# Kernel tuning notes

Hardware: AMD Instinct MI355X
Metric: run time of the kernel (lower is better)

Reference implementation:

```python
import jax, jax.numpy as jnp
import numpy as np

B, N, K, HID, L, OUT, HEADS = 2, 512, 30, 128, 3, 400, 4
FF = 4 * HID


def gather_nodes(nodes, idx):
    # nodes [B,N,C], idx [B,N,K] -> [B,N,K,C]
    return jax.vmap(lambda n, i: n[i])(nodes, idx)


def cat_edge_endpoints(h_E, h_V, E_idx):
    # h_i uses E_idx[:,:,0] (self node) broadcast over K, h_j gathers neighbors
    idx_i = jnp.broadcast_to(E_idx[:, :, :1], E_idx.shape)
    h_i = gather_nodes(h_V, idx_i)
    h_j = gather_nodes(h_V, E_idx)
    return jnp.concatenate([h_i, h_j, h_E], axis=-1)  # [B,N,K,3*HID]


def norm(x, g, b, eps=1e-6):
    # Ingraham-style Normalize: unbiased var, eps added to sigma too
    mu = x.mean(-1, keepdims=True)
    sigma = jnp.sqrt(x.var(-1, keepdims=True, ddof=1) + eps)
    return g * (x - mu) / (sigma + eps) + b


def edge_attention(h_E, h_EV, wq, wk, wv, wo, mask_attend):
    b, n, k, H = h_E.shape
    d = H // HEADS
    Q = (h_E @ wq).reshape(b, n, k, HEADS, d).transpose(0, 1, 3, 2, 4)   # [B,N,h,K,d]
    Kk = (h_EV @ wk).reshape(b, n, k, HEADS, d).transpose(0, 1, 3, 2, 4)
    Vv = (h_EV @ wv).reshape(b, n, k, HEADS, d).transpose(0, 1, 3, 2, 4)
    logits = jnp.einsum('bnhqd,bnhkd->bnhqk', Q, Kk) / np.float32(np.sqrt(d))
    m = mask_attend[:, :, None, :, None]                 # [B,N,1,K,1]
    mask = m * jnp.swapaxes(m, -1, -2)                   # [B,N,1,K,K]
    logits = jnp.where(mask > 0, logits, jnp.finfo(jnp.float32).min)
    attend = jax.nn.softmax(logits, axis=-1) * mask
    upd = jnp.einsum('bnhqk,bnhkd->bnhqd', attend, Vv)
    upd = upd.transpose(0, 1, 3, 2, 4).reshape(b, n, k, H)
    return upd @ wo


def merge_duplicate_edges(hE, E_idx):
    # scatter edges into dense [B,N,N,H], transpose, gather reverse edge, average
    b, n, k, h = hE.shape
    bi = jnp.arange(b)[:, None, None]
    ni = jnp.arange(n)[None, :, None]
    coll = jnp.zeros((b, n, n, h), hE.dtype).at[bi, ni, E_idx].set(hE)
    rev = coll.transpose(0, 2, 1, 3)[bi, ni, E_idx]
    return (hE + rev) / 2


def setup_inputs() -> dict:
    key = jax.random.key(0)
    ks = iter(jax.random.split(key, 32))

    def xav(k, shape):
        fan_in, fan_out = shape[-2], shape[-1]
        return jax.random.normal(k, shape, jnp.float32) * np.float32(np.sqrt(2.0 / (fan_in + fan_out)))

    V = jax.random.normal(next(ks), (B, N, HID), jnp.float32)
    E = jax.random.normal(next(ks), (B, N, K, HID), jnp.float32)
    x_mask = jnp.ones((B, N), jnp.float32)
    E_idx = jax.random.randint(next(ks), (B, N, K), 0, N)
    # slot 0 is the self edge, as in k-NN graphs
    E_idx = E_idx.at[:, :, 0].set(jnp.arange(N)[None, :])
    inp = dict(V=V, E=E, x_mask=x_mask, E_idx=E_idx)
    inp['Wv_w'] = xav(next(ks), (HID, HID)); inp['Wv_b'] = jnp.zeros((HID,), jnp.float32)
    inp['We_w'] = xav(next(ks), (HID, HID)); inp['We_b'] = jnp.zeros((HID,), jnp.float32)
    inp['WQ'] = xav(next(ks), (L, HID, HID))
    inp['WK'] = xav(next(ks), (L, 3 * HID, HID))
    inp['WV'] = xav(next(ks), (L, 3 * HID, HID))
    inp['WO'] = xav(next(ks), (L, HID, HID))
    inp['ln1_g'] = jnp.ones((L, HID), jnp.float32); inp['ln1_b'] = jnp.zeros((L, HID), jnp.float32)
    inp['ln2_g'] = jnp.ones((L, HID), jnp.float32); inp['ln2_b'] = jnp.zeros((L, HID), jnp.float32)
    inp['ff1_w'] = xav(next(ks), (L, HID, FF)); inp['ff1_b'] = jnp.zeros((L, FF), jnp.float32)
    inp['ff2_w'] = xav(next(ks), (L, FF, HID)); inp['ff2_b'] = jnp.zeros((L, HID), jnp.float32)
    inp['Wout_w'] = xav(next(ks), (HID, OUT)); inp['Wout_b'] = jnp.zeros((OUT,), jnp.float32)
    return inp


def reference(V, E, x_mask, E_idx, Wv_w, Wv_b, We_w, We_b, WQ, WK, WV, WO,
              ln1_g, ln1_b, ln2_g, ln2_b, ff1_w, ff1_b, ff2_w, ff2_b,
              Wout_w, Wout_b):
    h_V = V @ Wv_w + Wv_b                                   # [B,N,HID]
    h_E = E @ We_w + We_b                                   # [B,N,K,HID]
    mask_attend = gather_nodes(x_mask[..., None], E_idx)[..., 0] * x_mask[..., None]
    for l in range(L):
        h_EV = cat_edge_endpoints(h_E, h_V, E_idx)          # [B,N,K,3*HID]
        dh = edge_attention(h_E, h_EV, WQ[l], WK[l], WV[l], WO[l], mask_attend)
        h_E = norm(h_E + dh, ln1_g[l], ln1_b[l])
        dh = jnp.maximum(h_E @ ff1_w[l] + ff1_b[l], 0.0) @ ff2_w[l] + ff2_b[l]
        h_E = norm(h_E + dh, ln2_g[l], ln2_b[l])
        h_E = h_E * x_mask[:, :, None, None]                # mask_E
    h_out = h_E @ Wout_w + Wout_b                           # [B,N,K,OUT]
    return merge_duplicate_edges(h_out, E_idx)
```

## Files before the change

### kernel.cpp

```cpp
#include <hip/hip_runtime.h>

#define NB 512
#define KNB 30
#define HID 128
#define NL 3
#define NOUT 400
#define NFF 512

typedef _Float16 f16;
typedef _Float16 f16x8 __attribute__((ext_vector_type(8)));
typedef _Float16 f16x4 __attribute__((ext_vector_type(4)));
typedef float f32x4 __attribute__((ext_vector_type(4)));

#define MFMA16(a, b, c) __builtin_amdgcn_mfma_f32_16x16x32_f16(a, b, c, 0, 0, 0)

#define PK_WE   0
#define PK_WQ   16384
#define PK_WK   65536
#define PK_WV   114688
#define PK_WO   163840
#define PK_F1   212992
#define PK_F2   409600
#define PK_WOUT 606208
#define PK_TOTAL 657408

__global__ void k_hv(const float* __restrict__ V, const float* __restrict__ Wv,
                     const float* __restrict__ bv, float* __restrict__ hV) {
  int idx = blockIdx.x * 256 + threadIdx.x;
  int row = idx >> 7, c = idx & 127;
  const float* vr = V + row * HID;
  float acc = bv[c];
  for (int i = 0; i < HID; ++i) acc = fmaf(vr[i], Wv[i * HID + c], acc);
  hV[idx] = acc;
}

__global__ void k_tables(const float* __restrict__ hV, const float* __restrict__ WK,
                         const float* __restrict__ WVp, float* __restrict__ tbl) {
  int idx = blockIdx.x * 256 + threadIdx.x;
  int c = idx & 127;
  int row = (idx >> 7) & 1023;
  int t = idx >> 17;
  int l = t >> 2, part = t & 3;
  const float* W;
  if (part == 0)      W = WK  + l * 3 * HID * HID;
  else if (part == 1) W = WK  + l * 3 * HID * HID + HID * HID;
  else if (part == 2) W = WVp + l * 3 * HID * HID;
  else                W = WVp + l * 3 * HID * HID + HID * HID;
  const float* hr = hV + row * HID;
  float acc = 0.f;
  for (int i = 0; i < HID; ++i) acc = fmaf(hr[i], W[i * HID + c], acc);
  tbl[idx] = acc;
}

__device__ __forceinline__ void pack_one(const float* W, int N, int r, f16* dst) {
  int j = r & 7, l = (r >> 3) & 63, t = r >> 9;
  int NT = N >> 4;
  int nt = t % NT, ks = t / NT;
  int k = ks * 32 + ((l >> 4) << 3) + j;
  int c = nt * 16 + (l & 15);
  dst[r] = (f16)W[k * N + c];
}

__global__ void k_pack(const float* __restrict__ We, const float* __restrict__ WQ,
                       const float* __restrict__ WK, const float* __restrict__ WV,
                       const float* __restrict__ WO, const float* __restrict__ f1w,
                       const float* __restrict__ f2w, const float* __restrict__ Wout,
                       f16* __restrict__ P) {
  int idx = blockIdx.x * 256 + threadIdx.x;
  if (idx >= PK_TOTAL) return;
  const float* W; int N; int r; f16* dst;
  if (idx < 212992) {
    int s = idx >> 14; r = idx & 16383; N = 128;
    dst = P + (idx - r);
    if (s == 0) W = We;
    else if (s < 4) W = WQ + (s - 1) * 16384;
    else if (s < 7) W = WK + (s - 4) * 49152 + 32768;
    else if (s < 10) W = WV + (s - 7) * 49152 + 32768;
    else W = WO + (s - 10) * 16384;
  } else if (idx < 409600) {
    int t = (idx - 212992) >> 16; r = (idx - 212992) & 65535;
    W = f1w + t * 65536; N = 512; dst = P + 212992 + t * 65536;
  } else if (idx < 606208) {
    int t = (idx - 409600) >> 16; r = (idx - 409600) & 65535;
    W = f2w + t * 65536; N = 128; dst = P + 409600 + t * 65536;
  } else {
    r = idx - 606208; W = Wout; N = 400; dst = P + 606208;
  }
  pack_one(W, N, r, dst);
}

__device__ __forceinline__ void mfma_block8(const f16* Ab, int astr, const f16x8* B,
                                            int nt0, int nt1, f32x4 acc[2][2],
                                            int ln, int g, int lane) {
  f16x8 af[2][4];
#pragma unroll
  for (int mt = 0; mt < 2; ++mt)
#pragma unroll
    for (int ks = 0; ks < 4; ++ks)
      af[mt][ks] = *(const f16x8*)&Ab[(mt * 16 + ln) * astr + ks * 32 + g * 8];
#pragma unroll
  for (int ks = 0; ks < 4; ++ks) {
    f16x8 b0 = B[(ks * 8 + nt0) * 64 + lane];
    f16x8 b1 = B[(ks * 8 + nt1) * 64 + lane];
#pragma unroll
    for (int mt = 0; mt < 2; ++mt) {
      acc[mt][0] = MFMA16(af[mt][ks], b0, acc[mt][0]);
      acc[mt][1] = MFMA16(af[mt][ks], b1, acc[mt][1]);
    }
  }
}

__device__ __forceinline__ void layer_norm_cvt(float (*hEp)[132], f16* hEhp,
                                               const float* __restrict__ gg,
                                               const float* __restrict__ bb,
                                               float mmul, int tid) {
  int r = tid >> 3, g8 = tid & 7;
  if (r < KNB) {
    float x[16]; float s1 = 0.f, s2 = 0.f;
    int cb = g8 * 16;
#pragma unroll
    for (int m = 0; m < 16; ++m) { x[m] = hEp[r][cb + m]; s1 += x[m]; s2 += x[m] * x[m]; }
#pragma unroll
    for (int o = 1; o < 8; o <<= 1) { s1 += __shfl_xor(s1, o); s2 += __shfl_xor(s2, o); }
    float mu = s1 * (1.f / 128.f);
    float var = fmaf(-s1, mu, s2) * (1.f / 127.f);
    float inv = 1.f / (sqrtf(var + 1e-6f) + 1e-6f);
    f16x8 h0, h1;
#pragma unroll
    for (int m = 0; m < 16; ++m) {
      int c = cb + m;
      float y = (gg[c] * (x[m] - mu) * inv + bb[c]) * mmul;
      hEp[r][c] = y;
      if (m < 8) h0[m] = (f16)y; else h1[m - 8] = (f16)y;
    }
    *(f16x8*)&hEhp[r * 136 + cb] = h0;
    *(f16x8*)&hEhp[r * 136 + cb + 8] = h1;
  }
}

__launch_bounds__(256, 2)
__global__ void k_main(
    const float* __restrict__ E, const int* __restrict__ Eix, const float* __restrict__ xm,
    const float* __restrict__ be,
    const float* __restrict__ l1g, const float* __restrict__ l1b,
    const float* __restrict__ l2g, const float* __restrict__ l2b,
    const float* __restrict__ f1b, const float* __restrict__ f2b,
    const float* __restrict__ bout,
    const f16* __restrict__ P, const float* __restrict__ tbl,
    float* __restrict__ gOUT) {
  __shared__ __align__(16) char SM[63744];
  float (*hE)[132] = (float(*)[132])SM;
  f16* hEh = (f16*)(SM + 16896);
  char* poolB = SM + 25600;
  f16* Qh   = (f16*)(poolB);
  f16* Kh   = (f16*)(poolB + 8704);
  f16* Vt   = (f16*)(poolB + 17408);
  f16* atth = (f16*)(poolB + 27648);
  f16* hidh = (f16*)(poolB);
  float* ma = (float*)(SM + 63488);
  int* eidx = (int*)(SM + 63616);

  const int tid = threadIdx.x;
  const int bid = blockIdx.x;
  const int b = bid >> 9, n = bid & (NB - 1);
  const int lane = tid & 63, wv = tid >> 6;
  const int ln = lane & 15, g = lane >> 4;

  {
    float4 z = make_float4(0.f, 0.f, 0.f, 0.f);
    float4* p = (float4*)(SM + 16896);
    for (int x = tid; x < 2912; x += 256) p[x] = z;
  }
  if (tid < 32) {
    int e = (tid < KNB) ? Eix[(b * NB + n) * KNB + tid] : 0;
    eidx[tid] = e;
    float mr = xm[b * NB + n];
    ma[tid] = (tid < KNB) ? mr * xm[b * NB + e] : 0.f;
  }
  __syncthreads();
  {
    const float4* Eg = (const float4*)(E + (size_t)(b * NB + n) * KNB * HID);
    for (int x = tid; x < 960; x += 256) {
      float4 e4 = Eg[x];
      int r = x >> 5, c = (x & 31) << 2;
      f16x4 h; h[0] = (f16)e4.x; h[1] = (f16)e4.y; h[2] = (f16)e4.z; h[3] = (f16)e4.w;
      *(f16x4*)&hEh[r * 136 + c] = h;
    }
  }
  const float mrow = xm[b * NB + n];
  __syncthreads();

  {
    f32x4 acc[2][2] = {};
    mfma_block8(hEh, 136, (const f16x8*)(P + PK_WE), wv, wv + 4, acc, ln, g, lane);
    __syncthreads();
#pragma unroll
    for (int nts = 0; nts < 2; ++nts) {
      int c = (wv + nts * 4) * 16 + ln;
      float bev = be[c];
#pragma unroll
      for (int mt = 0; mt < 2; ++mt)
#pragma unroll
        for (int i = 0; i < 4; ++i) {
          int r = mt * 16 + 4 * g + i;
          if (r < KNB) {
            float v = acc[mt][nts][i] + bev;
            hE[r][c] = v;
            hEh[r * 136 + c] = (f16)v;
          }
        }
    }
  }
  __syncthreads();

  for (int l = 0; l < NL; ++l) {
    const f16x8* PQ = (const f16x8*)(P + PK_WQ + l * 16384);
    const f16x8* PKk = (const f16x8*)(P + PK_WK + l * 16384);
    const f16x8* PV = (const f16x8*)(P + PK_WV + l * 16384);
    const f16x8* PO = (const f16x8*)(P + PK_WO + l * 16384);
    const f16x8* P1 = (const f16x8*)(P + PK_F1 + l * 65536);
    const f16x8* P2 = (const f16x8*)(P + PK_F2 + l * 65536);
    const float* Ki = tbl + (size_t)(l * 4 + 0) * (2 * NB * HID) + (size_t)b * NB * HID;
    const float* Kj = tbl + (size_t)(l * 4 + 1) * (2 * NB * HID) + (size_t)b * NB * HID;
    const float* Vi = tbl + (size_t)(l * 4 + 2) * (2 * NB * HID) + (size_t)b * NB * HID;
    const float* Vj = tbl + (size_t)(l * 4 + 3) * (2 * NB * HID) + (size_t)b * NB * HID;

    {
      int e0v = eidx[0];
      int er[2][4];
#pragma unroll
      for (int mt = 0; mt < 2; ++mt)
#pragma unroll
        for (int i = 0; i < 4; ++i) er[mt][i] = eidx[mt * 16 + 4 * g + i];
      float kib[2], vib[2], kjv[2][2][4], vjv[2][2][4];
#pragma unroll
      for (int nts = 0; nts < 2; ++nts) {
        int c = (wv + nts * 4) * 16 + ln;
        kib[nts] = Ki[e0v * 128 + c];
        vib[nts] = Vi[e0v * 128 + c];
#pragma unroll
        for (int mt = 0; mt < 2; ++mt)
#pragma unroll
          for (int i = 0; i < 4; ++i) {
            kjv[nts][mt][i] = Kj[er[mt][i] * 128 + c];
            vjv[nts][mt][i] = Vj[er[mt][i] * 128 + c];
          }
      }
      f32x4 qa[2][2] = {}, kk[2][2] = {}, va[2][2] = {};
      mfma_block8(hEh, 136, PQ, wv, wv + 4, qa, ln, g, lane);
      mfma_block8(hEh, 136, PKk, wv, wv + 4, kk, ln, g, lane);
      mfma_block8(hEh, 136, PV, wv, wv + 4, va, ln, g, lane);
#pragma unroll
      for (int nts = 0; nts < 2; ++nts) {
        int c = (wv + nts * 4) * 16 + ln;
#pragma unroll
        for (int mt = 0; mt < 2; ++mt)
#pragma unroll
          for (int i = 0; i < 4; ++i) {
            int r = mt * 16 + 4 * g + i;
            Qh[r * 136 + c] = (f16)qa[mt][nts][i];
            Kh[r * 136 + c] = (f16)(kk[mt][nts][i] + kib[nts] + kjv[nts][mt][i]);
            Vt[c * 40 + r]  = (f16)(va[mt][nts][i] + vib[nts] + vjv[nts][mt][i]);
          }
      }
    }
    __syncthreads();

    {
      int h = wv;
      f16* ath = atth + h * 1280;
      f16x8 qf[2], kf[2];
#pragma unroll
      for (int mt = 0; mt < 2; ++mt)
        qf[mt] = *(const f16x8*)&Qh[(mt * 16 + ln) * 136 + h * 32 + g * 8];
#pragma unroll
      for (int nt = 0; nt < 2; ++nt)
        kf[nt] = *(const f16x8*)&Kh[(nt * 16 + ln) * 136 + h * 32 + g * 8];
      f32x4 s[2][2] = {};
#pragma unroll
      for (int mt = 0; mt < 2; ++mt)
#pragma unroll
        for (int nt = 0; nt < 2; ++nt) s[mt][nt] = MFMA16(qf[mt], kf[nt], s[mt][nt]);
      float mk0 = ma[ln], mk1 = ma[16 + ln];
      const float scale = 0.17677669529663687f;
#pragma unroll
      for (int mt = 0; mt < 2; ++mt) {
#pragma unroll
        for (int i = 0; i < 4; ++i) {
          int q = mt * 16 + 4 * g + i;
          float mq = ma[q];
          float v0 = s[mt][0][i] * scale;
          float v1 = s[mt][1][i] * scale;
          v0 = (mq * mk0 > 0.f) ? v0 : -3.4028234663852886e38f;
          v1 = (mq * mk1 > 0.f) ? v1 : -3.4028234663852886e38f;
          float mx = fmaxf(v0, v1);
          mx = fmaxf(mx, __shfl_xor(mx, 1));
          mx = fmaxf(mx, __shfl_xor(mx, 2));
          mx = fmaxf(mx, __shfl_xor(mx, 4));
          mx = fmaxf(mx, __shfl_xor(mx, 8));
          float e0 = __expf(v0 - mx), e1 = __expf(v1 - mx);
          float sm = e0 + e1;
          sm += __shfl_xor(sm, 1); sm += __shfl_xor(sm, 2);
          sm += __shfl_xor(sm, 4); sm += __shfl_xor(sm, 8);
          float inv = 1.f / sm;
          ath[q * 40 + ln]      = (f16)(e0 * inv * (mq * mk0));
          ath[q * 40 + 16 + ln] = (f16)(e1 * inv * (mq * mk1));
        }
      }
      asm volatile("s_waitcnt lgkmcnt(0)" ::: "memory");
      __builtin_amdgcn_sched_barrier(0);
      f32x4 u[2][2] = {};
      f16x8 aat[2], vbf[2];
#pragma unroll
      for (int mt = 0; mt < 2; ++mt)
        aat[mt] = *(const f16x8*)&ath[(mt * 16 + ln) * 40 + g * 8];
#pragma unroll
      for (int nt = 0; nt < 2; ++nt)
        vbf[nt] = *(const f16x8*)&Vt[((2 * h + nt) * 16 + ln) * 40 + g * 8];
#pragma unroll
      for (int mt = 0; mt < 2; ++mt)
#pragma unroll
        for (int nt = 0; nt < 2; ++nt) u[mt][nt] = MFMA16(aat[mt], vbf[nt], u[mt][nt]);
#pragma unroll
      for (int mt = 0; mt < 2; ++mt)
#pragma unroll
        for (int nt = 0; nt < 2; ++nt)
#pragma unroll
          for (int i = 0; i < 4; ++i) {
            int r = mt * 16 + 4 * g + i;
            hEh[r * 136 + h * 32 + nt * 16 + ln] = (f16)u[mt][nt][i];
          }
    }
    __syncthreads();

    {
      f32x4 acc[2][2] = {};
      mfma_block8(hEh, 136, PO, wv, wv + 4, acc, ln, g, lane);
#pragma unroll
      for (int nts = 0; nts < 2; ++nts) {
        int c = (wv + nts * 4) * 16 + ln;
#pragma unroll
        for (int mt = 0; mt < 2; ++mt)
#pragma unroll
          for (int i = 0; i < 4; ++i) {
            int r = mt * 16 + 4 * g + i;
            if (r < KNB) hE[r][c] += acc[mt][nts][i];
          }
      }
    }
    __syncthreads();
    layer_norm_cvt(hE, hEh, l1g + l * HID, l1b + l * HID, 1.f, tid);
    __syncthreads();

    {
      f16x8 af[2][4];
#pragma unroll
      for (int mt = 0; mt < 2; ++mt)
#pragma unroll
        for (int ks = 0; ks < 4; ++ks)
          af[mt][ks] = *(const f16x8*)&hEh[(mt * 16 + ln) * 136 + ks * 32 + g * 8];
      f32x4 acc[2][8] = {};
#pragma unroll
      for (int ks = 0; ks < 4; ++ks)
#pragma unroll
        for (int t = 0; t < 8; ++t) {
          f16x8 bv = P1[(ks * 32 + wv + 4 * t) * 64 + lane];
          acc[0][t] = MFMA16(af[0][ks], bv, acc[0][t]);
          acc[1][t] = MFMA16(af[1][ks], bv, acc[1][t]);
        }
      const float* b1 = f1b + l * NFF;
#pragma unroll
      for (int t = 0; t < 8; ++t) {
        int c = (wv + 4 * t) * 16 + ln;
        float b1v = b1[c];
#pragma unroll
        for (int mt = 0; mt < 2; ++mt)
#pragma unroll
          for (int i = 0; i < 4; ++i) {
            int r = mt * 16 + 4 * g + i;
            hidh[r * 520 + c] = (f16)fmaxf(acc[mt][t][i] + b1v, 0.f);
          }
      }
    }
    __syncthreads();

    {
      f32x4 acc[2][2] = {};
#pragma unroll
      for (int ks = 0; ks < 16; ++ks) {
        f16x8 a0 = *(const f16x8*)&hidh[ln * 520 + ks * 32 + g * 8];
        f16x8 a1 = *(const f16x8*)&hidh[(16 + ln) * 520 + ks * 32 + g * 8];
        f16x8 b0 = P2[(ks * 8 + wv) * 64 + lane];
        f16x8 b1 = P2[(ks * 8 + wv + 4) * 64 + lane];
        acc[0][0] = MFMA16(a0, b0, acc[0][0]);
        acc[0][1] = MFMA16(a0, b1, acc[0][1]);
        acc[1][0] = MFMA16(a1, b0, acc[1][0]);
        acc[1][1] = MFMA16(a1, b1, acc[1][1]);
      }
      const float* b2 = f2b + l * HID;
#pragma unroll
      for (int nts = 0; nts < 2; ++nts) {
        int c = (wv + nts * 4) * 16 + ln;
        float b2v = b2[c];
#pragma unroll
        for (int mt = 0; mt < 2; ++mt)
#pragma unroll
          for (int i = 0; i < 4; ++i) {
            int r = mt * 16 + 4 * g + i;
            if (r < KNB) hE[r][c] += acc[mt][nts][i] + b2v;
          }
      }
    }
    __syncthreads();
    layer_norm_cvt(hE, hEh, l2g + l * HID, l2b + l * HID, mrow, tid);
    __syncthreads();
  }

  {
    float* gO = gOUT + (size_t)((b * NB + n) * KNB) * NOUT;
    f16x8 af[2][4];
#pragma unroll
    for (int mt = 0; mt < 2; ++mt)
#pragma unroll
      for (int ks = 0; ks < 4; ++ks)
        af[mt][ks] = *(const f16x8*)&hEh[(mt * 16 + ln) * 136 + ks * 32 + g * 8];
    const f16x8* PW = (const f16x8*)(P + PK_WOUT);
#pragma unroll
    for (int mt = 0; mt < 2; ++mt) {
      for (int nt = wv; nt < 25; nt += 4) {
        f32x4 acc = {};
#pragma unroll
        for (int ks = 0; ks < 4; ++ks) {
          f16x8 bv = PW[(ks * 25 + nt) * 64 + lane];
          acc = MFMA16(af[mt][ks], bv, acc);
        }
        int c = nt * 16 + ln;
        float bo = bout[c];
#pragma unroll
        for (int i = 0; i < 4; ++i) {
          int r = mt * 16 + 4 * g + i;
          if (r < KNB) gO[r * 400 + c] = acc[i] + bo;
        }
      }
    }
  }
}

__global__ void k_clearT(int* __restrict__ T) {
  int i = blockIdx.x * 256 + threadIdx.x;
  if (i < 2 * NB * NB) T[i] = 0;
}
__global__ void k_buildT(const int* __restrict__ Eix, int* __restrict__ T) {
  int idx = blockIdx.x * 256 + threadIdx.x;
  if (idx < 2 * NB * KNB) {
    int b = idx / (NB * KNB);
    int rem = idx % (NB * KNB);
    int i = rem / KNB, k = rem % KNB;
    int j = Eix[idx];
    atomicMax(&T[(b * NB + i) * NB + j], k + 1);
  }
}
__global__ void k_merge(const float* __restrict__ HO, const int* __restrict__ Eix,
                        const int* __restrict__ T, float* __restrict__ out) {
  int gid = blockIdx.x * 256 + threadIdx.x;
  if (gid >= 2 * NB * KNB * (NOUT / 4)) return;
  int c4 = gid % (NOUT / 4);
  int bnk = gid / (NOUT / 4);
  int b = bnk / (NB * KNB);
  int n = (bnk / KNB) % NB;
  int j = Eix[bnk];
  int kp = T[(b * NB + j) * NB + n];
  float4 a = ((const float4*)HO)[(size_t)bnk * (NOUT / 4) + c4];
  float4 rv = make_float4(0.f, 0.f, 0.f, 0.f);
  if (kp > 0) rv = ((const float4*)HO)[(size_t)((b * NB + j) * KNB + (kp - 1)) * (NOUT / 4) + c4];
  ((float4*)out)[gid] = make_float4(0.5f * (a.x + rv.x), 0.5f * (a.y + rv.y),
                                    0.5f * (a.z + rv.z), 0.5f * (a.w + rv.w));
}

extern "C" void kernel_launch(void* const* d_in, const int* in_sizes, int n_in,
                              void* d_out, int out_size, void* d_ws, size_t ws_size,
                              hipStream_t stream) {
  const float* V   = (const float*)d_in[0];
  const float* E   = (const float*)d_in[1];
  const float* xmk = (const float*)d_in[2];
  const int*   Eix = (const int*)d_in[3];
  const float* Wv  = (const float*)d_in[4];
  const float* bv  = (const float*)d_in[5];
  const float* We  = (const float*)d_in[6];
  const float* be  = (const float*)d_in[7];
  const float* WQ  = (const float*)d_in[8];
  const float* WK  = (const float*)d_in[9];
  const float* WVp = (const float*)d_in[10];
  const float* WO  = (const float*)d_in[11];
  const float* l1g = (const float*)d_in[12];
  const float* l1b = (const float*)d_in[13];
  const float* l2g = (const float*)d_in[14];
  const float* l2b = (const float*)d_in[15];
  const float* f1w = (const float*)d_in[16];
  const float* f1b = (const float*)d_in[17];
  const float* f2w = (const float*)d_in[18];
  const float* f2b = (const float*)d_in[19];
  const float* Wou = (const float*)d_in[20];
  const float* bou = (const float*)d_in[21];

  float* HO  = (float*)d_ws;
  float* tbl = HO + 12288000ull;
  float* hV  = tbl + 1572864ull;
  f16*   P   = (f16*)(hV + 131072ull);
  int*   T   = (int*)tbl;

  k_hv<<<512, 256, 0, stream>>>(V, Wv, bv, hV);
  k_tables<<<6144, 256, 0, stream>>>(hV, WK, WVp, tbl);
  k_pack<<<2568, 256, 0, stream>>>(We, WQ, WK, WVp, WO, f1w, f2w, Wou, P);
  k_main<<<1024, 256, 0, stream>>>(E, Eix, xmk, be, l1g, l1b, l2g, l2b,
                                   f1b, f2b, bou, P, tbl, HO);
  k_clearT<<<2048, 256, 0, stream>>>(T);
  k_buildT<<<120, 256, 0, stream>>>(Eix, T);
  k_merge<<<12000, 256, 0, stream>>>(HO, Eix, T, (float*)d_out);
}
```

Measured before the change: 342.7 us.

## Restructure k_main to two waves owning 16-row slabs with register-resident residual

Reworks the main edge kernel from 4 waves splitting output columns into 2 waves each owning 16 edge rows across all 128 columns. The residual stream now stays in registers and layer norm runs on those registers with shuffle reductions, which removes the fp32 shared-memory copy and most block barriers. The FFN is chunked so the 512-wide hidden layer is produced and consumed in 128-column pieces through a small per-wave buffer. The cost is fewer threads per block, higher register pressure, and each wave reloading every weight fragment, which may lower occupancy or raise global/L2 traffic.

Result: slower. 575.1 us (+67.8%).

```diff
diff --git a/kernel.cpp b/kernel.cpp
--- a/kernel.cpp
+++ b/kernel.cpp
@@ -13,6 +13,7 @@
 typedef float f32x4 __attribute__((ext_vector_type(4)));
 
 #define MFMA16(a, b, c) __builtin_amdgcn_mfma_f32_16x16x32_f16(a, b, c, 0, 0, 0)
+#define FLTMIN -3.4028234663852886e38f
 
 #define PK_WE   0
 #define PK_WQ   16384
@@ -89,56 +90,39 @@
   pack_one(W, N, r, dst);
 }
 
-__device__ __forceinline__ void mfma_block8(const f16* Ab, int astr, const f16x8* B,
-                                            int nt0, int nt1, f32x4 acc[2][2],
-                                            int ln, int g, int lane) {
-  f16x8 af[2][4];
-#pragma unroll
-  for (int mt = 0; mt < 2; ++mt)
-#pragma unroll
-    for (int ks = 0; ks < 4; ++ks)
-      af[mt][ks] = *(const f16x8*)&Ab[(mt * 16 + ln) * astr + ks * 32 + g * 8];
-#pragma unroll
-  for (int ks = 0; ks < 4; ++ks) {
-    f16x8 b0 = B[(ks * 8 + nt0) * 64 + lane];
-    f16x8 b1 = B[(ks * 8 + nt1) * 64 + lane];
-#pragma unroll
-    for (int mt = 0; mt < 2; ++mt) {
-      acc[mt][0] = MFMA16(af[mt][ks], b0, acc[mt][0]);
-      acc[mt][1] = MFMA16(af[mt][ks], b1, acc[mt][1]);
-    }
-  }
-}
-
-__device__ __forceinline__ void layer_norm_cvt(float (*hEp)[132], f16* hEhp,
-                                               const float* __restrict__ gg,
-                                               const float* __restrict__ bb,
-                                               float mmul, int tid) {
-  int r = tid >> 3, g8 = tid & 7;
-  if (r < KNB) {
-    float x[16]; float s1 = 0.f, s2 = 0.f;
-    int cb = g8 * 16;
-#pragma unroll
-    for (int m = 0; m < 16; ++m) { x[m] = hEp[r][cb + m]; s1 += x[m]; s2 += x[m] * x[m]; }
-#pragma unroll
-    for (int o = 1; o < 8; o <<= 1) { s1 += __shfl_xor(s1, o); s2 += __shfl_xor(s2, o); }
-    float mu = s1 * (1.f / 128.f);
-    float var = fmaf(-s1, mu, s2) * (1.f / 127.f);
-    float inv = 1.f / (sqrtf(var + 1e-6f) + 1e-6f);
-    f16x8 h0, h1;
-#pragma unroll
-    for (int m = 0; m < 16; ++m) {
-      int c = cb + m;
-      float y = (gg[c] * (x[m] - mu) * inv + bb[c]) * mmul;
-      hEp[r][c] = y;
-      if (m < 8) h0[m] = (f16)y; else h1[m - 8] = (f16)y;
-    }
-    *(f16x8*)&hEhp[r * 136 + cb] = h0;
-    *(f16x8*)&hEhp[r * 136 + cb + 8] = h1;
-  }
-}
-
-__launch_bounds__(256, 2)
+__device__ __forceinline__ void ln_regs(f32x4 res[8], const float* __restrict__ gp,
+                                        const float* __restrict__ bp, float mmul,
+                                        f16* hEhA, int ln, int g) {
+  float s1[4] = {0.f, 0.f, 0.f, 0.f}, s2[4] = {0.f, 0.f, 0.f, 0.f};
+#pragma unroll
+  for (int nt = 0; nt < 8; ++nt)
+#pragma unroll
+    for (int i = 0; i < 4; ++i) { float x = res[nt][i]; s1[i] += x; s2[i] += x * x; }
+#pragma unroll
+  for (int o = 1; o < 16; o <<= 1)
+#pragma unroll
+    for (int i = 0; i < 4; ++i) { s1[i] += __shfl_xor(s1[i], o); s2[i] += __shfl_xor(s2[i], o); }
+  float gl[8], bl[8];
+#pragma unroll
+  for (int nt = 0; nt < 8; ++nt) { gl[nt] = gp[nt * 16 + ln]; bl[nt] = bp[nt * 16 + ln]; }
+  float mu[4], inv[4];
+#pragma unroll
+  for (int i = 0; i < 4; ++i) {
+    mu[i] = s1[i] * (1.f / 128.f);
+    float var = fmaf(-s1[i], mu[i], s2[i]) * (1.f / 127.f);
+    inv[i] = 1.f / (sqrtf(var + 1e-6f) + 1e-6f);
+  }
+#pragma unroll
+  for (int nt = 0; nt < 8; ++nt)
+#pragma unroll
+    for (int i = 0; i < 4; ++i) {
+      float y = (gl[nt] * (res[nt][i] - mu[i]) * inv[i] + bl[nt]) * mmul;
+      res[nt][i] = y;
+      hEhA[(4 * g + i) * 136 + nt * 16 + ln] = (f16)y;
+    }
+}
+
+__launch_bounds__(128, 2)
 __global__ void k_main(
     const float* __restrict__ E, const int* __restrict__ Eix, const float* __restrict__ xm,
     const float* __restrict__ be,
@@ -148,70 +132,78 @@
     const float* __restrict__ bout,
     const f16* __restrict__ P, const float* __restrict__ tbl,
     float* __restrict__ gOUT) {
-  __shared__ __align__(16) char SM[63744];
-  float (*hE)[132] = (float(*)[132])SM;
-  f16* hEh = (f16*)(SM + 16896);
-  char* poolB = SM + 25600;
-  f16* Qh   = (f16*)(poolB);
-  f16* Kh   = (f16*)(poolB + 8704);
-  f16* Vt   = (f16*)(poolB + 17408);
-  f16* atth = (f16*)(poolB + 27648);
-  f16* hidh = (f16*)(poolB);
-  float* ma = (float*)(SM + 63488);
-  int* eidx = (int*)(SM + 63616);
+  __shared__ __align__(16) char SM[39040];
+  f16* Kh = (f16*)SM;
+  f16* Vt = (f16*)(SM + 8704);
+  float* ma = (float*)(SM + 18944);
 
   const int tid = threadIdx.x;
+  const int w = tid >> 6, lane = tid & 63, ln = lane & 15, g = lane >> 4;
+  f16* hEhA = (f16*)(SM + 19072 + w * 4352);
+  f16* Qh   = (f16*)(SM + 27776 + w * 5632);
+  f16* ath  = Qh + 2176;
+  f16* hidc = Qh;
+
   const int bid = blockIdx.x;
   const int b = bid >> 9, n = bid & (NB - 1);
-  const int lane = tid & 63, wv = tid >> 6;
-  const int ln = lane & 15, g = lane >> 4;
+  const int rb = w * 16;
+  const int ebase = (b * NB + n) * KNB;
+  const float mrow = xm[b * NB + n];
+
+  int rr[4], er[4];
+#pragma unroll
+  for (int i = 0; i < 4; ++i) {
+    rr[i] = rb + 4 * g + i;
+    er[i] = (rr[i] < KNB) ? Eix[ebase + rr[i]] : 0;
+  }
+  const int e0 = Eix[ebase];
+
+  if (w == 0 && lane < 32)
+    ma[lane] = (lane < KNB) ? mrow * xm[b * NB + Eix[ebase + lane]] : 0.f;
+
+  for (int x = lane; x < 512; x += 64) {
+    int lr = x >> 5, c4 = (x & 31) << 2;
+    int r = rb + lr;
+    f16x4 h4 = {};
+    if (r < KNB) {
+      float4 e4 = *(const float4*)(E + (size_t)ebase * HID + (size_t)r * HID + c4);
+      h4[0] = (f16)e4.x; h4[1] = (f16)e4.y; h4[2] = (f16)e4.z; h4[3] = (f16)e4.w;
+    }
+    *(f16x4*)&hEhA[lr * 136 + c4] = h4;
+  }
+
+  f32x4 res[8];
 
   {
-    float4 z = make_float4(0.f, 0.f, 0.f, 0.f);
-    float4* p = (float4*)(SM + 16896);
-    for (int x = tid; x < 2912; x += 256) p[x] = z;
-  }
-  if (tid < 32) {
-    int e = (tid < KNB) ? Eix[(b * NB + n) * KNB + tid] : 0;
-    eidx[tid] = e;
-    float mr = xm[b * NB + n];
-    ma[tid] = (tid < KNB) ? mr * xm[b * NB + e] : 0.f;
+    f16x8 af[4];
+#pragma unroll
+    for (int ks = 0; ks < 4; ++ks)
+      af[ks] = *(const f16x8*)&hEhA[ln * 136 + ks * 32 + g * 8];
+    f32x4 acc[8] = {};
+    const f16x8* PB = (const f16x8*)(P + PK_WE);
+#pragma unroll
+    for (int ks = 0; ks < 4; ++ks)
+#pragma unroll
+      for (int nt = 0; nt < 8; ++nt)
+        acc[nt] = MFMA16(af[ks], PB[(ks * 8 + nt) * 64 + lane], acc[nt]);
+#pragma unroll
+    for (int nt = 0; nt < 8; ++nt) {
+      float bev = be[nt * 16 + ln];
+#pragma unroll
+      for (int i = 0; i < 4; ++i) res[nt][i] = acc[nt][i] + bev;
+    }
+#pragma unroll
+    for (int nt = 0; nt < 8; ++nt)
+#pragma unroll
+      for (int i = 0; i < 4; ++i)
+        hEhA[(4 * g + i) * 136 + nt * 16 + ln] = (f16)res[nt][i];
   }
   __syncthreads();
-  {
-    const float4* Eg = (const float4*)(E + (size_t)(b * NB + n) * KNB * HID);
-    for (int x = tid; x < 960; x += 256) {
-      float4 e4 = Eg[x];
-      int r = x >> 5, c = (x & 31) << 2;
-      f16x4 h; h[0] = (f16)e4.x; h[1] = (f16)e4.y; h[2] = (f16)e4.z; h[3] = (f16)e4.w;
-      *(f16x4*)&hEh[r * 136 + c] = h;
-    }
-  }
-  const float mrow = xm[b * NB + n];
-  __syncthreads();
-
-  {
-    f32x4 acc[2][2] = {};
-    mfma_block8(hEh, 136, (const f16x8*)(P + PK_WE), wv, wv + 4, acc, ln, g, lane);
-    __syncthreads();
-#pragma unroll
-    for (int nts = 0; nts < 2; ++nts) {
-      int c = (wv + nts * 4) * 16 + ln;
-      float bev = be[c];
-#pragma unroll
-      for (int mt = 0; mt < 2; ++mt)
-#pragma unroll
-        for (int i = 0; i < 4; ++i) {
-          int r = mt * 16 + 4 * g + i;
-          if (r < KNB) {
-            float v = acc[mt][nts][i] + bev;
-            hE[r][c] = v;
-            hEh[r * 136 + c] = (f16)v;
-          }
-        }
-    }
-  }
-  __syncthreads();
+
+  float mam[4];
+#pragma unroll
+  for (int i = 0; i < 4; ++i) mam[i] = ma[rr[i] & 31];
+  const float mk0 = ma[ln], mk1 = ma[16 + ln];
 
   for (int l = 0; l < NL; ++l) {
     const f16x8* PQ = (const f16x8*)(P + PK_WQ + l * 16384);
@@ -225,223 +217,193 @@
     const float* Vi = tbl + (size_t)(l * 4 + 2) * (2 * NB * HID) + (size_t)b * NB * HID;
     const float* Vj = tbl + (size_t)(l * 4 + 3) * (2 * NB * HID) + (size_t)b * NB * HID;
 
+    float kib[8], vib[8], kjv[8][4], vjv[8][4];
+#pragma unroll
+    for (int nt = 0; nt < 8; ++nt) {
+      int c = nt * 16 + ln;
+      kib[nt] = Ki[e0 * HID + c];
+      vib[nt] = Vi[e0 * HID + c];
+#pragma unroll
+      for (int i = 0; i < 4; ++i) {
+        kjv[nt][i] = Kj[er[i] * HID + c];
+        vjv[nt][i] = Vj[er[i] * HID + c];
+      }
+    }
+
+    f16x8 af[4];
+#pragma unroll
+    for (int ks = 0; ks < 4; ++ks)
+      af[ks] = *(const f16x8*)&hEhA[ln * 136 + ks * 32 + g * 8];
+
     {
-      int e0v = eidx[0];
-      int er[2][4];
-#pragma unroll
-      for (int mt = 0; mt < 2; ++mt)
-#pragma unroll
-        for (int i = 0; i < 4; ++i) er[mt][i] = eidx[mt * 16 + 4 * g + i];
-      float kib[2], vib[2], kjv[2][2][4], vjv[2][2][4];
-#pragma unroll
-      for (int nts = 0; nts < 2; ++nts) {
-        int c = (wv + nts * 4) * 16 + ln;
-        kib[nts] = Ki[e0v * 128 + c];
-        vib[nts] = Vi[e0v * 128 + c];
-#pragma unroll
-        for (int mt = 0; mt < 2; ++mt)
-#pragma unroll
-          for (int i = 0; i < 4; ++i) {
-            kjv[nts][mt][i] = Kj[er[mt][i] * 128 + c];
-            vjv[nts][mt][i] = Vj[er[mt][i] * 128 + c];
-          }
-      }
-      f32x4 qa[2][2] = {}, kk[2][2] = {}, va[2][2] = {};
-      mfma_block8(hEh, 136, PQ, wv, wv + 4, qa, ln, g, lane);
-      mfma_block8(hEh, 136, PKk, wv, wv + 4, kk, ln, g, lane);
-      mfma_block8(hEh, 136, PV, wv, wv + 4, va, ln, g, lane);
-#pragma unroll
-      for (int nts = 0; nts < 2; ++nts) {
-        int c = (wv + nts * 4) * 16 + ln;
-#pragma unroll
-        for (int mt = 0; mt < 2; ++mt)
-#pragma unroll
-          for (int i = 0; i < 4; ++i) {
-            int r = mt * 16 + 4 * g + i;
-            Qh[r * 136 + c] = (f16)qa[mt][nts][i];
-            Kh[r * 136 + c] = (f16)(kk[mt][nts][i] + kib[nts] + kjv[nts][mt][i]);
-            Vt[c * 40 + r]  = (f16)(va[mt][nts][i] + vib[nts] + vjv[nts][mt][i]);
-          }
-      }
+      f32x4 acc[8] = {};
+#pragma unroll
+      for (int ks = 0; ks < 4; ++ks)
+#pragma unroll
+        for (int nt = 0; nt < 8; ++nt)
+          acc[nt] = MFMA16(af[ks], PQ[(ks * 8 + nt) * 64 + lane], acc[nt]);
+#pragma unroll
+      for (int nt = 0; nt < 8; ++nt)
+#pragma unroll
+        for (int i = 0; i < 4; ++i)
+          Qh[(4 * g + i) * 136 + nt * 16 + ln] = (f16)acc[nt][i];
+    }
+    {
+      f32x4 acc[8] = {};
+#pragma unroll
+      for (int ks = 0; ks < 4; ++ks)
+#pragma unroll
+        for (int nt = 0; nt < 8; ++nt)
+          acc[nt] = MFMA16(af[ks], PKk[(ks * 8 + nt) * 64 + lane], acc[nt]);
+#pragma unroll
+      for (int nt = 0; nt < 8; ++nt)
+#pragma unroll
+        for (int i = 0; i < 4; ++i)
+          Kh[(rb + 4 * g + i) * 136 + nt * 16 + ln] = (f16)(acc[nt][i] + kib[nt] + kjv[nt][i]);
+    }
+    {
+      f32x4 acc[8] = {};
+#pragma unroll
+      for (int ks = 0; ks < 4; ++ks)
+#pragma unroll
+        for (int nt = 0; nt < 8; ++nt)
+          acc[nt] = MFMA16(af[ks], PV[(ks * 8 + nt) * 64 + lane], acc[nt]);
+#pragma unroll
+      for (int nt = 0; nt < 8; ++nt)
+#pragma unroll
+        for (int i = 0; i < 4; ++i)
+          Vt[(nt * 16 + ln) * 40 + rb + 4 * g + i] = (f16)(acc[nt][i] + vib[nt] + vjv[nt][i]);
     }
     __syncthreads();
 
+    const float scale = 0.17677669529663687f;
+#pragma unroll
+    for (int h = 0; h < 4; ++h) {
+      f16x8 aq = *(const f16x8*)&Qh[ln * 136 + h * 32 + g * 8];
+      f16x8 bk0 = *(const f16x8*)&Kh[ln * 136 + h * 32 + g * 8];
+      f16x8 bk1 = *(const f16x8*)&Kh[(16 + ln) * 136 + h * 32 + g * 8];
+      f32x4 s0 = {}, s1v = {};
+      s0 = MFMA16(aq, bk0, s0);
+      s1v = MFMA16(aq, bk1, s1v);
+      float a0[4], a1[4];
+#pragma unroll
+      for (int i = 0; i < 4; ++i) {
+        float mq = mam[i];
+        float p0 = mq * mk0, p1 = mq * mk1;
+        float v0 = (p0 > 0.f) ? s0[i] * scale : FLTMIN;
+        float v1 = (p1 > 0.f) ? s1v[i] * scale : FLTMIN;
+        float mx = fmaxf(v0, v1);
+        mx = fmaxf(mx, __shfl_xor(mx, 1));
+        mx = fmaxf(mx, __shfl_xor(mx, 2));
+        mx = fmaxf(mx, __shfl_xor(mx, 4));
+        mx = fmaxf(mx, __shfl_xor(mx, 8));
+        float e0v = __expf(v0 - mx), e1v = __expf(v1 - mx);
+        float sm = e0v + e1v;
+        sm += __shfl_xor(sm, 1); sm += __shfl_xor(sm, 2);
+        sm += __shfl_xor(sm, 4); sm += __shfl_xor(sm, 8);
+        float iv = 1.f / sm;
+        a0[i] = e0v * iv * p0;
+        a1[i] = e1v * iv * p1;
+      }
+#pragma unroll
+      for (int i = 0; i < 4; ++i) {
+        ath[(4 * g + i) * 40 + ln] = (f16)a0[i];
+        ath[(4 * g + i) * 40 + 16 + ln] = (f16)a1[i];
+      }
+      f16x8 pa = *(const f16x8*)&ath[ln * 40 + g * 8];
+      f16x8 bv0 = *(const f16x8*)&Vt[(h * 32 + ln) * 40 + g * 8];
+      f16x8 bv1 = *(const f16x8*)&Vt[(h * 32 + 16 + ln) * 40 + g * 8];
+      f32x4 u0 = {}, u1 = {};
+      u0 = MFMA16(pa, bv0, u0);
+      u1 = MFMA16(pa, bv1, u1);
+#pragma unroll
+      for (int i = 0; i < 4; ++i) {
+        hEhA[(4 * g + i) * 136 + h * 32 + ln] = (f16)u0[i];
+        hEhA[(4 * g + i) * 136 + h * 32 + 16 + ln] = (f16)u1[i];
+      }
+    }
+    __syncthreads();
+
     {
-      int h = wv;
-      f16* ath = atth + h * 1280;
-      f16x8 qf[2], kf[2];
-#pragma unroll
-      for (int mt = 0; mt < 2; ++mt)
-        qf[mt] = *(const f16x8*)&Qh[(mt * 16 + ln) * 136 + h * 32 + g * 8];
-#pragma unroll
-      for (int nt = 0; nt < 2; ++nt)
-        kf[nt] = *(const f16x8*)&Kh[(nt * 16 + ln) * 136 + h * 32 + g * 8];
-      f32x4 s[2][2] = {};
-#pragma unroll
-      for (int mt = 0; mt < 2; ++mt)
-#pragma unroll
-        for (int nt = 0; nt < 2; ++nt) s[mt][nt] = MFMA16(qf[mt], kf[nt], s[mt][nt]);
-      float mk0 = ma[ln], mk1 = ma[16 + ln];
-      const float scale = 0.17677669529663687f;
-#pragma unroll
-      for (int mt = 0; mt < 2; ++mt) {
-#pragma unroll
-        for (int i = 0; i < 4; ++i) {
-          int q = mt * 16 + 4 * g + i;
-          float mq = ma[q];
-          float v0 = s[mt][0][i] * scale;
-          float v1 = s[mt][1][i] * scale;
-          v0 = (mq * mk0 > 0.f) ? v0 : -3.4028234663852886e38f;
-          v1 = (mq * mk1 > 0.f) ? v1 : -3.4028234663852886e38f;
-          float mx = fmaxf(v0, v1);
-          mx = fmaxf(mx, __shfl_xor(mx, 1));
-          mx = fmaxf(mx, __shfl_xor(mx, 2));
-          mx = fmaxf(mx, __shfl_xor(mx, 4));
-          mx = fmaxf(mx, __shfl_xor(mx, 8));
-          float e0 = __expf(v0 - mx), e1 = __expf(v1 - mx);
-          float sm = e0 + e1;
-          sm += __shfl_xor(sm, 1); sm += __shfl_xor(sm, 2);
-          sm += __shfl_xor(sm, 4); sm += __shfl_xor(sm, 8);
-          float inv = 1.f / sm;
-          ath[q * 40 + ln]      = (f16)(e0 * inv * (mq * mk0));
-          ath[q * 40 + 16 + ln] = (f16)(e1 * inv * (mq * mk1));
-        }
-      }
-      asm volatile("s_waitcnt lgkmcnt(0)" ::: "memory");
-      __builtin_amdgcn_sched_barrier(0);
-      f32x4 u[2][2] = {};
-      f16x8 aat[2], vbf[2];
-#pragma unroll
-      for (int mt = 0; mt < 2; ++mt)
-        aat[mt] = *(const f16x8*)&ath[(mt * 16 + ln) * 40 + g * 8];
-#pragma unroll
-      for (int nt = 0; nt < 2; ++nt)
-        vbf[nt] = *(const f16x8*)&Vt[((2 * h + nt) * 16 + ln) * 40 + g * 8];
-#pragma unroll
-      for (int mt = 0; mt < 2; ++mt)
-#pragma unroll
-        for (int nt = 0; nt < 2; ++nt) u[mt][nt] = MFMA16(aat[mt], vbf[nt], u[mt][nt]);
-#pragma unroll
-      for (int mt = 0; mt < 2; ++mt)
-#pragma unroll
-        for (int nt = 0; nt < 2; ++nt)
-#pragma unroll
-          for (int i = 0; i < 4; ++i) {
-            int r = mt * 16 + 4 * g + i;
-            hEh[r * 136 + h * 32 + nt * 16 + ln] = (f16)u[mt][nt][i];
-          }
-    }
-    __syncthreads();
+      f16x8 au[4];
+#pragma unroll
+      for (int ks = 0; ks < 4; ++ks)
+        au[ks] = *(const f16x8*)&hEhA[ln * 136 + ks * 32 + g * 8];
+      f32x4 acc[8] = {};
+#pragma unroll
+      for (int ks = 0; ks < 4; ++ks)
+#pragma unroll
+        for (int nt = 0; nt < 8; ++nt)
+          acc[nt] = MFMA16(au[ks], PO[(ks * 8 + nt) * 64 + lane], acc[nt]);
+#pragma unroll
+      for (int nt = 0; nt < 8; ++nt)
+#pragma unroll
+        for (int i = 0; i < 4; ++i) res[nt][i] += acc[nt][i];
+    }
+    ln_regs(res, l1g + l * HID, l1b + l * HID, 1.f, hEhA, ln, g);
 
     {
-      f32x4 acc[2][2] = {};
-      mfma_block8(hEh, 136, PO, wv, wv + 4, acc, ln, g, lane);
-#pragma unroll
-      for (int nts = 0; nts < 2; ++nts) {
-        int c = (wv + nts * 4) * 16 + ln;
-#pragma unroll
-        for (int mt = 0; mt < 2; ++mt)
-#pragma unroll
-          for (int i = 0; i < 4; ++i) {
-            int r = mt * 16 + 4 * g + i;
-            if (r < KNB) hE[r][c] += acc[mt][nts][i];
-          }
-      }
-    }
-    __syncthreads();
-    layer_norm_cvt(hE, hEh, l1g + l * HID, l1b + l * HID, 1.f, tid);
-    __syncthreads();
-
-    {
-      f16x8 af[2][4];
-#pragma unroll
-      for (int mt = 0; mt < 2; ++mt)
+      f16x8 aff[4];
+#pragma unroll
+      for (int ks = 0; ks < 4; ++ks)
+        aff[ks] = *(const f16x8*)&hEhA[ln * 136 + ks * 32 + g * 8];
+      f32x4 ff[8] = {};
+      const float* b1 = f1b + l * NFF;
+#pragma unroll
+      for (int ch = 0; ch < 4; ++ch) {
+        float b1v[8];
+#pragma unroll
+        for (int nt = 0; nt < 8; ++nt) b1v[nt] = b1[ch * 128 + nt * 16 + ln];
+        f32x4 h1[8] = {};
 #pragma unroll
         for (int ks = 0; ks < 4; ++ks)
-          af[mt][ks] = *(const f16x8*)&hEh[(mt * 16 + ln) * 136 + ks * 32 + g * 8];
-      f32x4 acc[2][8] = {};
-#pragma unroll
-      for (int ks = 0; ks < 4; ++ks)
-#pragma unroll
-        for (int t = 0; t < 8; ++t) {
-          f16x8 bv = P1[(ks * 32 + wv + 4 * t) * 64 + lane];
-          acc[0][t] = MFMA16(af[0][ks], bv, acc[0][t]);
-          acc[1][t] = MFMA16(af[1][ks], bv, acc[1][t]);
-        }
-      const float* b1 = f1b + l * NFF;
-#pragma unroll
-      for (int t = 0; t < 8; ++t) {
-        int c = (wv + 4 * t) * 16 + ln;
-        float b1v = b1[c];
-#pragma unroll
-        for (int mt = 0; mt < 2; ++mt)
-#pragma unroll
-          for (int i = 0; i < 4; ++i) {
-            int r = mt * 16 + 4 * g + i;
-            hidh[r * 520 + c] = (f16)fmaxf(acc[mt][t][i] + b1v, 0.f);
-          }
-      }
-    }
-    __syncthreads();
-
-    {
-      f32x4 acc[2][2] = {};
-#pragma unroll
-      for (int ks = 0; ks < 16; ++ks) {
-        f16x8 a0 = *(const f16x8*)&hidh[ln * 520 + ks * 32 + g * 8];
-        f16x8 a1 = *(const f16x8*)&hidh[(16 + ln) * 520 + ks * 32 + g * 8];
-        f16x8 b0 = P2[(ks * 8 + wv) * 64 + lane];
-        f16x8 b1 = P2[(ks * 8 + wv + 4) * 64 + lane];
-        acc[0][0] = MFMA16(a0, b0, acc[0][0]);
-        acc[0][1] = MFMA16(a0, b1, acc[0][1]);
-        acc[1][0] = MFMA16(a1, b0, acc[1][0]);
-        acc[1][1] = MFMA16(a1, b1, acc[1][1]);
+#pragma unroll
+          for (int nt = 0; nt < 8; ++nt)
+            h1[nt] = MFMA16(aff[ks], P1[(ks * 32 + ch * 8 + nt) * 64 + lane], h1[nt]);
+#pragma unroll
+        for (int nt = 0; nt < 8; ++nt)
+#pragma unroll
+          for (int i = 0; i < 4; ++i)
+            hidc[(4 * g + i) * 136 + nt * 16 + ln] = (f16)fmaxf(h1[nt][i] + b1v[nt], 0.f);
+        f16x8 ah[4];
+#pragma unroll
+        for (int k2 = 0; k2 < 4; ++k2)
+          ah[k2] = *(const f16x8*)&hidc[ln * 136 + k2 * 32 + g * 8];
+#pragma unroll
+        for (int k2 = 0; k2 < 4; ++k2)
+#pragma unroll
+          for (int nt = 0; nt < 8; ++nt)
+            ff[nt] = MFMA16(ah[k2], P2[((ch * 4 + k2) * 8 + nt) * 64 + lane], ff[nt]);
       }
       const float* b2 = f2b + l * HID;
 #pragma unroll
-      for (int nts = 0; nts < 2; ++nts) {
-        int c = (wv + nts * 4) * 16 + ln;
-        float b2v = b2[c];
-#pragma unroll
-        for (int mt = 0; mt < 2; ++mt)
-#pragma unroll
-          for (int i = 0; i < 4; ++i) {
-            int r = mt * 16 + 4 * g + i;
-            if (r < KNB) hE[r][c] += acc[mt][nts][i] + b2v;
-          }
-      }
-    }
-    __syncthreads();
-    layer_norm_cvt(hE, hEh, l2g + l * HID, l2b + l * HID, mrow, tid);
-    __syncthreads();
+      for (int nt = 0; nt < 8; ++nt) {
+        float b2v = b2[nt * 16 + ln];
+#pragma unroll
+        for (int i = 0; i < 4; ++i) res[nt][i] += ff[nt][i] + b2v;
+      }
+    }
+    ln_regs(res, l2g + l * HID, l2b + l * HID, mrow, hEhA, ln, g);
   }
 
   {
-    float* gO = gOUT + (size_t)((b * NB + n) * KNB) * NOUT;
-    f16x8 af[2][4];
-#pragma unroll
-    for (int mt = 0; mt < 2; ++mt)
-#pragma unroll
-      for (int ks = 0; ks < 4; ++ks)
-        af[mt][ks] = *(const f16x8*)&hEh[(mt * 16 + ln) * 136 + ks * 32 + g * 8];
+    float* gO = gOUT + (size_t)ebase * NOUT;
+    f16x8 af[4];
+#pragma unroll
+    for (int ks = 0; ks < 4; ++ks)
+      af[ks] = *(const f16x8*)&hEhA[ln * 136 + ks * 32 + g * 8];
     const f16x8* PW = (const f16x8*)(P + PK_WOUT);
-#pragma unroll
-    for (int mt = 0; mt < 2; ++mt) {
-      for (int nt = wv; nt < 25; nt += 4) {
-        f32x4 acc = {};
-#pragma unroll
-        for (int ks = 0; ks < 4; ++ks) {
-          f16x8 bv = PW[(ks * 25 + nt) * 64 + lane];
-          acc = MFMA16(af[mt][ks], bv, acc);
-        }
-        int c = nt * 16 + ln;
-        float bo = bout[c];
-#pragma unroll
-        for (int i = 0; i < 4; ++i) {
-          int r = mt * 16 + 4 * g + i;
-          if (r < KNB) gO[r * 400 + c] = acc[i] + bo;
-        }
-      }
+#pragma unroll 5
+    for (int nt = 0; nt < 25; ++nt) {
+      f32x4 acc = {};
+#pragma unroll
+      for (int ks = 0; ks < 4; ++ks)
+        acc = MFMA16(af[ks], PW[(ks * 25 + nt) * 64 + lane], acc);
+      int c = nt * 16 + ln;
+      float bo = bout[c];
+#pragma unroll
+      for (int i = 0; i < 4; ++i)
+        if (rr[i] < KNB) gO[(size_t)rr[i] * NOUT + c] = acc[i] + bo;
     }
   }
 }
@@ -512,7 +474,7 @@
   k_hv<<<512, 256, 0, stream>>>(V, Wv, bv, hV);
   k_tables<<<6144, 256, 0, stream>>>(hV, WK, WVp, tbl);
   k_pack<<<2568, 256, 0, stream>>>(We, WQ, WK, WVp, WO, f1w, f2w, Wou, P);
-  k_main<<<1024, 256, 0, stream>>>(E, Eix, xmk, be, l1g, l1b, l2g, l2b,
+  k_main<<<1024, 128, 0, stream>>>(E, Eix, xmk, be, l1g, l1b, l2g, l2b,
                                    f1b, f2b, bou, P, tbl, HO);
   k_clearT<<<2048, 256, 0, stream>>>(T);
   k_buildT<<<120, 256, 0, stream>>>(Eix, T);
```
